# Optimization experiments

Measured on AMD Instinct MI355X. Metric: run time of the kernel, lower is better.

The kernel has to match this reference:

```python
import jax, jax.numpy as jnp
import numpy as np
import math

N, E = 8192, 32768
MUL_S, MUL_V = 32, 16          # 32x0e + 16x1o
DIM = MUL_S + 3 * MUL_V        # 80
NUM_RBF, HID = 16, 64
CUTOFF = 5.0
ALPHA = 5.0 / CUTOFF
# per-edge TP weight sizes (uvw paths): ss->s, s sh1->v, v sh0->v, vv->s, vv->v
O1 = MUL_S * MUL_S              # 1024
O2 = O1 + MUL_S * MUL_V         # 1536
O3 = O2 + MUL_V * MUL_V         # 1792
O4 = O3 + MUL_V * MUL_S         # 2304
WNUM = O4 + MUL_V * MUL_V       # 2560


def setup_inputs() -> dict:
    key = jax.random.key(0)
    ks = jax.random.split(key, 8)
    h = jax.random.normal(ks[0], (N, DIM), jnp.float32)
    pos = jax.random.normal(ks[1], (N, 3), jnp.float32)
    edge_index = jax.random.randint(ks[2], (2, E), 0, N)
    start = math.exp(-CUTOFF)
    means = jnp.linspace(start, 1.0, NUM_RBF).astype(jnp.float32)
    betas = jnp.full((NUM_RBF,), (2.0 / NUM_RBF * (1.0 - start)) ** -2, jnp.float32)
    W1 = jax.random.normal(ks[3], (NUM_RBF, HID), jnp.float32) / np.sqrt(NUM_RBF).astype(np.float32)
    b1 = jnp.zeros((HID,), jnp.float32)
    W2 = jax.random.normal(ks[4], (HID, WNUM), jnp.float32) / np.sqrt(HID).astype(np.float32)
    b2 = jnp.zeros((WNUM,), jnp.float32)
    Wss = jax.random.normal(ks[5], (MUL_S, MUL_S), jnp.float32)
    Wvv = jax.random.normal(ks[6], (MUL_V, MUL_V), jnp.float32)
    return {"h": h, "pos": pos, "edge_index": edge_index, "means": means,
            "betas": betas, "W1": W1, "b1": b1, "W2": W2, "b2": b2,
            "Wss": Wss, "Wvv": Wvv}


def reference(h, pos, edge_index, means, betas, W1, b1, W2, b2, Wss, Wvv):
    src, dst = edge_index[0], edge_index[1]
    vec = pos[dst] - pos[src]                           # [E,3]
    d = jnp.sqrt(jnp.sum(vec * vec, -1) + 1e-12)        # [E]
    y1 = math.sqrt(3.0) * vec / d[:, None]              # l=1 SH, component norm
    # ExpNormalSmearing with cosine cutoff
    cut = 0.5 * (jnp.cos(d * math.pi / CUTOFF) + 1.0) * (d < CUTOFF).astype(h.dtype)
    expd = jnp.exp(-ALPHA * d)[:, None]
    rbf = jnp.exp(-betas * (expd - means) ** 2) * cut[:, None]   # [E,NUM_RBF]
    # edge MLP -> per-edge TP weights
    ew = jax.nn.silu(rbf @ W1 + b1) @ W2 + b2            # [E,WNUM]
    w_ss = ew[:, :O1].reshape(E, MUL_S, MUL_S)
    w_sv = ew[:, O1:O2].reshape(E, MUL_S, MUL_V)
    w_vs = ew[:, O2:O3].reshape(E, MUL_V, MUL_V)
    w_vv0 = ew[:, O3:O4].reshape(E, MUL_V, MUL_S)
    w_vv1 = ew[:, O4:].reshape(E, MUL_V, MUL_V)
    hs = h[:, :MUL_S]                                    # [N,32]
    hv = h[:, MUL_S:].reshape(N, MUL_V, 3)               # [N,16,3]
    s_src = hs[src]                                      # [E,32]
    v_src = hv[src]                                      # [E,16,3]
    # scalar outputs: (0e x 0e -> 0e) + (1o x 1o -> 0e)
    p1 = jnp.einsum('eu,euw->ew', s_src, w_ss)
    dot = jnp.einsum('eud,ed->eu', v_src, y1) / math.sqrt(3.0)
    p4 = jnp.einsum('eu,euw->ew', dot, w_vv0)
    out_s = (p1 / math.sqrt(MUL_S) + p4 / math.sqrt(MUL_V)) / math.sqrt(2.0)
    # vector outputs: (0e x 1o -> 1o) + (1o x 0e -> 1o) + (1o x 1o -> 1o)
    p2 = jnp.einsum('eu,euw,ed->ewd', s_src, w_sv, y1)
    p3 = jnp.einsum('eud,euw->ewd', v_src, w_vs)
    cross = jnp.cross(v_src, y1[:, None, :]) / math.sqrt(2.0)
    p5 = jnp.einsum('eud,euw->ewd', cross, w_vv1)
    out_v = (p2 / math.sqrt(MUL_S) + p3 / math.sqrt(MUL_V) + p5 / math.sqrt(MUL_V)) / math.sqrt(3.0)
    msgs = jnp.concatenate([out_s, out_v.reshape(E, 3 * MUL_V)], -1)   # [E,80]
    # scatter-mean to destination nodes
    agg = jax.ops.segment_sum(msgs, dst, num_segments=N)
    cnt = jax.ops.segment_sum(jnp.ones((E,), msgs.dtype), dst, num_segments=N)
    agg = agg / jnp.maximum(cnt, 1.0)[:, None]
    # equivariant self-interaction (per-irrep channel mixing)
    si_s = hs @ Wss / math.sqrt(MUL_S)
    si_v = jnp.einsum('nud,uw->nwd', hv, Wvv) / math.sqrt(MUL_V)
    self_i = jnp.concatenate([si_s, si_v.reshape(N, 3 * MUL_V)], -1)
    return agg + self_i + h   # residual
```

## Files before the change

kernel.cpp:

```cpp
#include <hip/hip_runtime.h>
#include <math.h>

#define NN 8192
#define EE 32768
#define WN 2560
#define HID_STRIDE 72

typedef unsigned short u16;
typedef unsigned int u32;
typedef short short8 __attribute__((ext_vector_type(8)));
typedef float f32x4 __attribute__((ext_vector_type(4)));

__device__ __forceinline__ u16 f2b(float f) {
    u32 x = __float_as_uint(f);
    return (u16)((x + 0x7fffu + ((x >> 16) & 1u)) >> 16);
}

__global__ __launch_bounds__(256) void prep(const float* __restrict__ W2,
                                            u16* __restrict__ W2T,
                                            float* __restrict__ zbase) {
    const int t = threadIdx.x, b = blockIdx.x;
    const float4 z4 = {0.f, 0.f, 0.f, 0.f};
    #pragma unroll
    for (int k = 0; k < 3; ++k) {
        int i = b * 768 + k * 256 + t;
        if (i < 165888) ((float4*)zbase)[i] = z4;
    }
    if (b < 40) {
        __shared__ float tile[64][65];
        const int c0 = b << 6;
        const int tl = t & 63, th = t >> 6;
        #pragma unroll
        for (int r = 0; r < 16; ++r) {
            int kk = (r << 2) + th;
            tile[kk][tl] = W2[kk * WN + c0 + tl];
        }
        __syncthreads();
        #pragma unroll
        for (int r = 0; r < 16; ++r) {
            int c = (r << 2) + th;
            W2T[(size_t)(c0 + c) * 64 + tl] = f2b(tile[tl][c]);
        }
    }
}

__global__ __launch_bounds__(256, 2) void edge_kernel(
    const float* __restrict__ h, const float* __restrict__ pos, const int* __restrict__ ei,
    const float* __restrict__ means, const float* __restrict__ betas,
    const float* __restrict__ W1, const float* __restrict__ b1,
    const u16* __restrict__ W2T, const float* __restrict__ b2,
    float* __restrict__ agg, float* __restrict__ cnt)
{
    __shared__ alignas(16) char sbuf[50688];
    float (*sh_ss)[33]    = (float (*)[33])(sbuf);
    float (*sh_dot)[17]   = (float (*)[17])(sbuf + 4224);
    float (*sh_v)[68]     = (float (*)[68])(sbuf + 6400);
    float (*sh_cross)[68] = (float (*)[68])(sbuf + 15104);
    u16*  sh_hidb         = (u16*)(sbuf + 23808);
    float (*redS)[32][33] = (float (*)[32][33])(sbuf);
    float (*redQ)[32][17] = (float (*)[32][17])(sbuf + 16896);
    float (*redV)[32][49] = (float (*)[32][49])(sbuf + 25600);

    __shared__ float sh_y1[32][3];
    __shared__ float sh_geo[32][2];
    __shared__ int   sh_src[32];
    __shared__ int   sh_dst[32];

    const int t = threadIdx.x;

    if (t < 32) {
        const int eg = (blockIdx.x << 5) + t;
        const int si = ei[eg];
        const int di = ei[EE + eg];
        float ax = pos[si*3+0], ay = pos[si*3+1], az = pos[si*3+2];
        float bx = pos[di*3+0], by = pos[di*3+1], bz = pos[di*3+2];
        float vx = bx-ax, vy = by-ay, vz = bz-az;
        float d = sqrtf(vx*vx + vy*vy + vz*vz + 1e-12f);
        float invd = 1.7320508075688772f / d;
        sh_y1[t][0] = vx*invd; sh_y1[t][1] = vy*invd; sh_y1[t][2] = vz*invd;
        sh_geo[t][0] = expf(-d);
        sh_geo[t][1] = (d < 5.0f) ? 0.5f*(cosf(d*0.6283185307179586f) + 1.0f) : 0.0f;
        sh_src[t] = si; sh_dst[t] = di;
    }
    __syncthreads();

    {
        const int e = t >> 3, r = t & 7;
        const float expd = sh_geo[e][0], cut = sh_geo[e][1];
        float rbf[16];
        #pragma unroll
        for (int k = 0; k < 16; ++k) {
            float td = expd - means[k];
            rbf[k] = expf(-betas[k]*td*td) * cut;
        }
        short8 pk;
        #pragma unroll
        for (int jj = 0; jj < 8; ++jj) {
            int j = (r << 3) + jj;
            float a = b1[j];
            #pragma unroll
            for (int k = 0; k < 16; ++k) a += rbf[k] * W1[(k<<6) + j];
            float s = a / (1.0f + expf(-a));
            pk[jj] = (short)f2b(s);
        }
        *(short8*)&sh_hidb[e*HID_STRIDE + (r<<3)] = pk;

        const int srcn = sh_src[e];
        const float* hrow = h + srcn*80;
        const float y1x = sh_y1[e][0], y1y = sh_y1[e][1], y1z = sh_y1[e][2];
        #pragma unroll
        for (int i = 0; i < 4; ++i) { int u = (r<<2)+i; sh_ss[e][u] = 0.125f * hrow[u]; }
        #pragma unroll
        for (int i = 0; i < 2; ++i) {
            int u = (r<<1)+i;
            float v0 = hrow[32+u*3+0];
            float v1 = hrow[32+u*3+1];
            float v2 = hrow[32+u*3+2];
            sh_v[e][(u<<2)+0] = v0 * 0.14433756729740643f;
            sh_v[e][(u<<2)+1] = v1 * 0.14433756729740643f;
            sh_v[e][(u<<2)+2] = v2 * 0.14433756729740643f;
            sh_dot[e][u] = (v0*y1x + v1*y1y + v2*y1z) * 0.10206207261596574f;
            sh_cross[e][(u<<2)+0] = (v1*y1z - v2*y1y) * 0.10206207261596574f;
            sh_cross[e][(u<<2)+1] = (v2*y1x - v0*y1z) * 0.10206207261596574f;
            sh_cross[e][(u<<2)+2] = (v0*y1y - v1*y1x) * 0.10206207261596574f;
        }
    }
    __syncthreads();

    const int ln = t & 63, wv = t >> 6;
    const int quad = ln >> 4, lm = ln & 15;
    short8 af[2][2];
    #pragma unroll
    for (int mt = 0; mt < 2; ++mt)
        #pragma unroll
        for (int ks = 0; ks < 2; ++ks)
            af[mt][ks] = *(const short8*)&sh_hidb[(mt*16+lm)*HID_STRIDE + (ks<<5) + (quad<<3)];

    float accS[2][4][2];
    float accQ[2][4];
    float accV[2][4][3];
    #pragma unroll
    for (int mt = 0; mt < 2; ++mt)
        #pragma unroll
        for (int r = 0; r < 4; ++r) {
            accS[mt][r][0] = accS[mt][r][1] = 0.f;
            accQ[mt][r] = 0.f;
            accV[mt][r][0] = accV[mt][r][1] = accV[mt][r][2] = 0.f;
        }

    #pragma unroll
    for (int ci = 0; ci < 10; ++ci) {
        short8 bfr[4][2];
        float b2v[4];
        #pragma unroll
        for (int i = 0; i < 4; ++i) {
            const int coll = (((wv<<2)+i)<<4) + lm;
            const int col  = (ci<<8) + coll;
            bfr[i][0] = *(const short8*)(W2T + (size_t)col*64 + (quad<<3));
            bfr[i][1] = *(const short8*)(W2T + (size_t)col*64 + 32 + (quad<<3));
            b2v[i] = b2[col];
        }
        f32x4 d[4][2];
        #pragma unroll
        for (int i = 0; i < 4; ++i) {
            d[i][0] = (f32x4){0.f,0.f,0.f,0.f};
            d[i][1] = (f32x4){0.f,0.f,0.f,0.f};
            d[i][0] = __builtin_amdgcn_mfma_f32_16x16x32_bf16(af[0][0], bfr[i][0], d[i][0], 0,0,0);
            d[i][0] = __builtin_amdgcn_mfma_f32_16x16x32_bf16(af[0][1], bfr[i][1], d[i][0], 0,0,0);
            d[i][1] = __builtin_amdgcn_mfma_f32_16x16x32_bf16(af[1][0], bfr[i][0], d[i][1], 0,0,0);
            d[i][1] = __builtin_amdgcn_mfma_f32_16x16x32_bf16(af[1][1], bfr[i][1], d[i][1], 0,0,0);
            d[i][0] += b2v[i];
            d[i][1] += b2v[i];
        }

        if (ci < 4) {
            const int ub = (ci<<3) + (wv<<1);
            #pragma unroll
            for (int mt = 0; mt < 2; ++mt)
                #pragma unroll
                for (int r = 0; r < 4; ++r) {
                    const int e = (mt<<4) + (quad<<2) + r;
                    float s0 = sh_ss[e][ub], s1 = sh_ss[e][ub+1];
                    accS[mt][r][0] += s0*d[0][mt][r] + s1*d[2][mt][r];
                    accS[mt][r][1] += s0*d[1][mt][r] + s1*d[3][mt][r];
                }
        } else if (ci < 6) {
            const int ub = ((ci-4)<<4) + (wv<<2);
            #pragma unroll
            for (int mt = 0; mt < 2; ++mt)
                #pragma unroll
                for (int r = 0; r < 4; ++r) {
                    const int e = (mt<<4) + (quad<<2) + r;
                    float a = 0.f;
                    #pragma unroll
                    for (int i = 0; i < 4; ++i) a += sh_ss[e][ub+i] * d[i][mt][r];
                    accQ[mt][r] += a;
                }
        } else if (ci == 6) {
            const int ub = wv << 2;
            #pragma unroll
            for (int mt = 0; mt < 2; ++mt)
                #pragma unroll
                for (int r = 0; r < 4; ++r) {
                    const int e = (mt<<4) + (quad<<2) + r;
                    #pragma unroll
                    for (int i = 0; i < 4; ++i) {
                        const float4 vv = *(const float4*)&sh_v[e][(ub+i)<<2];
                        float ew = d[i][mt][r];
                        accV[mt][r][0] += vv.x * ew;
                        accV[mt][r][1] += vv.y * ew;
                        accV[mt][r][2] += vv.z * ew;
                    }
                }
        } else if (ci < 9) {
            const int ub = ((ci-7)<<3) + (wv<<1);
            #pragma unroll
            for (int mt = 0; mt < 2; ++mt)
                #pragma unroll
                for (int r = 0; r < 4; ++r) {
                    const int e = (mt<<4) + (quad<<2) + r;
                    float s0 = sh_dot[e][ub], s1 = sh_dot[e][ub+1];
                    accS[mt][r][0] += s0*d[0][mt][r] + s1*d[2][mt][r];
                    accS[mt][r][1] += s0*d[1][mt][r] + s1*d[3][mt][r];
                }
        } else {
            const int ub = wv << 2;
            #pragma unroll
            for (int mt = 0; mt < 2; ++mt)
                #pragma unroll
                for (int r = 0; r < 4; ++r) {
                    const int e = (mt<<4) + (quad<<2) + r;
                    #pragma unroll
                    for (int i = 0; i < 4; ++i) {
                        const float4 cc = *(const float4*)&sh_cross[e][(ub+i)<<2];
                        float ew = d[i][mt][r];
                        accV[mt][r][0] += cc.x * ew;
                        accV[mt][r][1] += cc.y * ew;
                        accV[mt][r][2] += cc.z * ew;
                    }
                }
        }
    }

    __syncthreads();

    #pragma unroll
    for (int mt = 0; mt < 2; ++mt)
        #pragma unroll
        for (int r = 0; r < 4; ++r) {
            const int e = (mt<<4) + (quad<<2) + r;
            redS[wv][e][lm]      = accS[mt][r][0];
            redS[wv][e][lm+16]   = accS[mt][r][1];
            redQ[wv][e][lm]      = accQ[mt][r];
            redV[wv][e][lm*3+0]  = accV[mt][r][0];
            redV[wv][e][lm*3+1]  = accV[mt][r][1];
            redV[wv][e][lm*3+2]  = accV[mt][r][2];
        }
    __syncthreads();

    #pragma unroll
    for (int k = 0; k < 4; ++k) {
        int p = t + (k<<8); int e = p >> 5; int w = p & 31;
        float v = redS[0][e][w] + redS[1][e][w] + redS[2][e][w] + redS[3][e][w];
        atomicAdd(&agg[sh_dst[e]*80 + w], v);
    }
    #pragma unroll
    for (int k = 0; k < 6; ++k) {
        int p = t + (k<<8); int e = p/48; int m = p - e*48; int w = m/3; int dd = m - w*3;
        float pv = redV[0][e][m] + redV[1][e][m] + redV[2][e][m] + redV[3][e][m];
        float q2 = redQ[0][e][w] + redQ[1][e][w] + redQ[2][e][w] + redQ[3][e][w];
        float val = pv + q2 * sh_y1[e][dd] * 0.8164965809277261f;
        atomicAdd(&agg[sh_dst[e]*80 + 32 + m], val);
    }
    if (t < 32) atomicAdd(&cnt[sh_dst[t]], 1.0f);
}

__global__ __launch_bounds__(256, 4) void node_kernel(
    const float* __restrict__ h, const float* __restrict__ Wss, const float* __restrict__ Wvv,
    const float* __restrict__ agg, const float* __restrict__ cnt,
    float* __restrict__ out)
{
    const int idx = blockIdx.x*256 + threadIdx.x;
    const int n = idx / 80;
    const int j = idx - n*80;
    float a = agg[idx] / fmaxf(cnt[n], 1.0f);
    const float* hrow = h + n*80;
    float si = 0.f;
    if (j < 32) {
        #pragma unroll
        for (int u = 0; u < 32; ++u) si += hrow[u] * Wss[(u<<5)+j];
        si *= 0.17677669529663687f;
    } else {
        int m = j - 32; int w = m/3; int d = m - w*3;
        #pragma unroll
        for (int u = 0; u < 16; ++u) si += hrow[32+u*3+d] * Wvv[(u<<4)+w];
        si *= 0.25f;
    }
    out[idx] = a + si + hrow[j];
}

extern "C" void kernel_launch(void* const* d_in, const int* in_sizes, int n_in,
                              void* d_out, int out_size, void* d_ws, size_t ws_size,
                              hipStream_t stream) {
    const float* h     = (const float*)d_in[0];
    const float* pos   = (const float*)d_in[1];
    const int*   ei    = (const int*)d_in[2];
    const float* means = (const float*)d_in[3];
    const float* betas = (const float*)d_in[4];
    const float* W1    = (const float*)d_in[5];
    const float* b1    = (const float*)d_in[6];
    const float* W2    = (const float*)d_in[7];
    const float* b2    = (const float*)d_in[8];
    const float* Wss   = (const float*)d_in[9];
    const float* Wvv   = (const float*)d_in[10];

    float* agg = (float*)d_ws;
    float* cnt = agg + (size_t)NN*80;
    u16*   W2T = (u16*)(cnt + NN);

    hipLaunchKernelGGL(prep, dim3(256), dim3(256), 0, stream, W2, W2T, agg);
    hipLaunchKernelGGL(edge_kernel, dim3(EE/32), dim3(256), 0, stream,
                       h, pos, ei, means, betas, W1, b1, W2T, b2, agg, cnt);
    hipLaunchKernelGGL(node_kernel, dim3((NN*80)/256), dim3(256), 0, stream,
                       h, Wss, Wvv, agg, cnt, (float*)d_out);
}
```

Baseline: 141.9 us.

## Shrink edge kernel LDS via staged reduction and split node kernel by irrep

The edge kernel's cross-warp reduction now runs in two phases: scalar and dot partials are reduced first, then the vector partials reuse the same shared buffer. This cuts shared memory from about 50KB to about 28KB and raises the launch-bounds occupancy target from 2 to 4 blocks. The node kernel is split into separate block ranges for scalar and vector channels, which removes warp divergence between the two branches. The cost is one extra block barrier in the edge kernel and possible register pressure at the higher occupancy target.

```diff
diff --git a/kernel.cpp b/kernel.cpp
--- a/kernel.cpp
+++ b/kernel.cpp
@@ -44,14 +44,14 @@
     }
 }
 
-__global__ __launch_bounds__(256, 2) void edge_kernel(
+__global__ __launch_bounds__(256, 4) void edge_kernel(
     const float* __restrict__ h, const float* __restrict__ pos, const int* __restrict__ ei,
     const float* __restrict__ means, const float* __restrict__ betas,
     const float* __restrict__ W1, const float* __restrict__ b1,
     const u16* __restrict__ W2T, const float* __restrict__ b2,
     float* __restrict__ agg, float* __restrict__ cnt)
 {
-    __shared__ alignas(16) char sbuf[50688];
+    __shared__ alignas(16) char sbuf[28416];
     float (*sh_ss)[33]    = (float (*)[33])(sbuf);
     float (*sh_dot)[17]   = (float (*)[17])(sbuf + 4224);
     float (*sh_v)[68]     = (float (*)[68])(sbuf + 6400);
@@ -59,7 +59,7 @@
     u16*  sh_hidb         = (u16*)(sbuf + 23808);
     float (*redS)[32][33] = (float (*)[32][33])(sbuf);
     float (*redQ)[32][17] = (float (*)[32][17])(sbuf + 16896);
-    float (*redV)[32][49] = (float (*)[32][49])(sbuf + 25600);
+    float (*redV)[32][49] = (float (*)[32][49])(sbuf);
 
     __shared__ float sh_y1[32][3];
     __shared__ float sh_geo[32][2];
@@ -243,18 +243,14 @@
     }
 
     __syncthreads();
-
     #pragma unroll
     for (int mt = 0; mt < 2; ++mt)
         #pragma unroll
         for (int r = 0; r < 4; ++r) {
             const int e = (mt<<4) + (quad<<2) + r;
-            redS[wv][e][lm]      = accS[mt][r][0];
-            redS[wv][e][lm+16]   = accS[mt][r][1];
-            redQ[wv][e][lm]      = accQ[mt][r];
-            redV[wv][e][lm*3+0]  = accV[mt][r][0];
-            redV[wv][e][lm*3+1]  = accV[mt][r][1];
-            redV[wv][e][lm*3+2]  = accV[mt][r][2];
+            redS[wv][e][lm]    = accS[mt][r][0];
+            redS[wv][e][lm+16] = accS[mt][r][1];
+            redQ[wv][e][lm]    = accQ[mt][r];
         }
     __syncthreads();
 
@@ -264,39 +260,65 @@
         float v = redS[0][e][w] + redS[1][e][w] + redS[2][e][w] + redS[3][e][w];
         atomicAdd(&agg[sh_dst[e]*80 + w], v);
     }
-    #pragma unroll
-    for (int k = 0; k < 6; ++k) {
-        int p = t + (k<<8); int e = p/48; int m = p - e*48; int w = m/3; int dd = m - w*3;
-        float pv = redV[0][e][m] + redV[1][e][m] + redV[2][e][m] + redV[3][e][m];
-        float q2 = redQ[0][e][w] + redQ[1][e][w] + redQ[2][e][w] + redQ[3][e][w];
-        float val = pv + q2 * sh_y1[e][dd] * 0.8164965809277261f;
-        atomicAdd(&agg[sh_dst[e]*80 + 32 + m], val);
+    float q2v[2];
+    #pragma unroll
+    for (int k = 0; k < 2; ++k) {
+        int p = t + (k<<8); int e = p >> 4; int w = p & 15;
+        q2v[k] = redQ[0][e][w] + redQ[1][e][w] + redQ[2][e][w] + redQ[3][e][w];
+    }
+    __syncthreads();
+
+    #pragma unroll
+    for (int mt = 0; mt < 2; ++mt)
+        #pragma unroll
+        for (int r = 0; r < 4; ++r) {
+            const int e = (mt<<4) + (quad<<2) + r;
+            redV[wv][e][lm*3+0] = accV[mt][r][0];
+            redV[wv][e][lm*3+1] = accV[mt][r][1];
+            redV[wv][e][lm*3+2] = accV[mt][r][2];
+        }
+    __syncthreads();
+
+    #pragma unroll
+    for (int k = 0; k < 2; ++k) {
+        int p = t + (k<<8); int e = p >> 4; int w = p & 15;
+        #pragma unroll
+        for (int dd = 0; dd < 3; ++dd) {
+            int m = w*3 + dd;
+            float pv = redV[0][e][m] + redV[1][e][m] + redV[2][e][m] + redV[3][e][m];
+            float val = pv + q2v[k] * sh_y1[e][dd] * 0.8164965809277261f;
+            atomicAdd(&agg[sh_dst[e]*80 + 32 + m], val);
+        }
     }
     if (t < 32) atomicAdd(&cnt[sh_dst[t]], 1.0f);
 }
 
-__global__ __launch_bounds__(256, 4) void node_kernel(
+__global__ __launch_bounds__(256, 8) void node_kernel(
     const float* __restrict__ h, const float* __restrict__ Wss, const float* __restrict__ Wvv,
     const float* __restrict__ agg, const float* __restrict__ cnt,
     float* __restrict__ out)
 {
-    const int idx = blockIdx.x*256 + threadIdx.x;
-    const int n = idx / 80;
-    const int j = idx - n*80;
-    float a = agg[idx] / fmaxf(cnt[n], 1.0f);
-    const float* hrow = h + n*80;
-    float si = 0.f;
-    if (j < 32) {
+    const int b = blockIdx.x, t = threadIdx.x;
+    if (b < 1024) {
+        const int idx = (b<<8) + t;
+        const int n = idx >> 5, j = idx & 31;
+        const float* hrow = h + n*80;
+        float si = 0.f;
         #pragma unroll
         for (int u = 0; u < 32; ++u) si += hrow[u] * Wss[(u<<5)+j];
-        si *= 0.17677669529663687f;
+        float a = agg[n*80+j] / fmaxf(cnt[n], 1.0f);
+        out[n*80+j] = a + si*0.17677669529663687f + hrow[j];
     } else {
-        int m = j - 32; int w = m/3; int d = m - w*3;
+        const int idx = ((b-1024)<<8) + t;
+        const int n = idx / 48, m = idx - n*48;
+        const int w = m/3, d = m - w*3;
+        const float* hrow = h + n*80;
+        float si = 0.f;
         #pragma unroll
         for (int u = 0; u < 16; ++u) si += hrow[32+u*3+d] * Wvv[(u<<4)+w];
-        si *= 0.25f;
-    }
-    out[idx] = a + si + hrow[j];
+        float a = agg[n*80+32+m] / fmaxf(cnt[n], 1.0f);
+        out[n*80+32+m] = a + si*0.25f + hrow[32+m];
+    }
 }
 
 extern "C" void kernel_launch(void* const* d_in, const int* in_sizes, int n_in,
@@ -321,6 +343,6 @@
     hipLaunchKernelGGL(prep, dim3(256), dim3(256), 0, stream, W2, W2T, agg);
     hipLaunchKernelGGL(edge_kernel, dim3(EE/32), dim3(256), 0, stream,
                        h, pos, ei, means, betas, W1, b1, W2T, b2, agg, cnt);
-    hipLaunchKernelGGL(node_kernel, dim3((NN*80)/256), dim3(256), 0, stream,
+    hipLaunchKernelGGL(node_kernel, dim3(2560), dim3(256), 0, stream,
                        h, Wss, Wvv, agg, cnt, (float*)d_out);
 }
```

New measurement: 184.2 us. +29.8%, slower.
